# Kernel tuning notes

Hardware: AMD Instinct MI355X
Metric: run time of the kernel (lower is better)

Reference implementation:

```python
import jax, jax.numpy as jnp
import numpy as np
import math

D_MODEL = 768
NUM_HEADS = 12
SPARSITY = 0.7


def setup_inputs() -> dict:
    key = jax.random.key(0)
    ks = jax.random.split(key, 9)
    B, S, D = 2, 2048, D_MODEL
    scale = 1.0 / math.sqrt(D)  # xavier-ish
    inp = {
        "x": jax.random.normal(ks[0], (B, S, D), dtype=jnp.float32),
        "Wq": jax.random.normal(ks[1], (D, D), dtype=jnp.float32) * scale,
        "bq": jnp.zeros((D,), dtype=jnp.float32),
        "Wk": jax.random.normal(ks[2], (D, D), dtype=jnp.float32) * scale,
        "bk": jnp.zeros((D,), dtype=jnp.float32),
        "Wv": jax.random.normal(ks[3], (D, D), dtype=jnp.float32) * scale,
        "bv": jnp.zeros((D,), dtype=jnp.float32),
        "Wo": jax.random.normal(ks[4], (D, D), dtype=jnp.float32) * scale,
        "bo": jnp.zeros((D,), dtype=jnp.float32),
    }
    return inp


def reference(x, Wq, bq, Wk, bk, Wv, bv, Wo, bo):
    B, S, D = x.shape
    H = NUM_HEADS
    hd = D // H
    k_keep = max(1, int((1.0 - SPARSITY) * S))

    # projections (nn.Linear: x @ W.T + b), split into heads -> [B,H,S,hd]
    q = (x @ Wq.T + bq).reshape(B, S, H, hd).transpose(0, 2, 1, 3)
    k = (x @ Wk.T + bk).reshape(B, S, H, hd).transpose(0, 2, 1, 3)
    v = (x @ Wv.T + bv).reshape(B, S, H, hd).transpose(0, 2, 1, 3)

    # dense scores [B,H,S,S]
    scores = jnp.einsum("bhqd,bhkd->bhqk", q, k) / math.sqrt(hd)

    # per-row top-k sparsification (training path of the torch module)
    _, topk_idx = jax.lax.top_k(scores, k_keep)  # [B,H,S,k]
    bi = jnp.arange(B)[:, None, None, None]
    hi = jnp.arange(H)[None, :, None, None]
    si = jnp.arange(S)[None, None, :, None]
    keep = jnp.zeros(scores.shape, dtype=bool).at[bi, hi, si, topk_idx].set(True)
    scores = jnp.where(keep, scores, jnp.float32(-1e9))

    attn = jax.nn.softmax(scores, axis=-1)
    out = jnp.einsum("bhqk,bhkd->bhqd", attn, v)  # [B,H,S,hd]
    out = out.transpose(0, 2, 1, 3).reshape(B, S, D)
    return out @ Wo.T + bo
```

## Files before the change

kernel.cpp:

```cpp
#include <hip/hip_runtime.h>
#include <math.h>

#define B_ 2
#define S_ 2048
#define D_ 768
#define H_ 12
#define HD_ 64
#define KKEEP 614
#define M_ (B_*S_)
#define KD_ 768
#define SRW 2072

typedef __attribute__((ext_vector_type(8))) short bf8;
typedef __attribute__((ext_vector_type(4))) float f4;

__device__ __forceinline__ unsigned short f2bf(float f) {
    unsigned u = __float_as_uint(f);
    u += 0x7FFF + ((u >> 16) & 1);
    return (unsigned short)(u >> 16);
}
__device__ __forceinline__ float bf2f(unsigned short h) {
    return __uint_as_float((unsigned)h << 16);
}
__device__ __forceinline__ unsigned ord16(unsigned short h) {
    return (h & 0x8000u) ? ((~(unsigned)h) & 0xFFFFu) : ((unsigned)h | 0x8000u);
}
__device__ __forceinline__ unsigned short inv16(unsigned o) {
    return (unsigned short)((o & 0x8000u) ? (o & 0x7FFFu) : ((~o) & 0xFFFFu));
}

__global__ void split_kernel(const float* __restrict__ src,
                             unsigned short* __restrict__ hi,
                             unsigned short* __restrict__ lo, int n) {
    int i = blockIdx.x * blockDim.x + threadIdx.x;
    int stride = gridDim.x * blockDim.x;
    for (; i < n; i += stride) {
        float f = src[i];
        unsigned short h = f2bf(f);
        hi[i] = h;
        lo[i] = f2bf(f - bf2f(h));
    }
}

template<int MODE, int WLO>
__global__ __launch_bounds__(256)
void gemm_bf16s(const unsigned short* __restrict__ Ahi, const unsigned short* __restrict__ Alo,
                const unsigned short* __restrict__ Whi, const unsigned short* __restrict__ Wlo,
                const float* __restrict__ bias,
                float* __restrict__ outf,
                unsigned short* __restrict__ ohi, unsigned short* __restrict__ olo) {
    __shared__ unsigned short Ah[128][32], Al[128][32], Bh[64][32], Bl[64][32];
    const int bm = blockIdx.x * 128, bn = blockIdx.y * 64;
    const int tid = threadIdx.x, lane = tid & 63, wave = tid >> 6;
    const int col = lane & 15, quad = lane >> 4;

    f4 acc[2][4];
#pragma unroll
    for (int mi = 0; mi < 2; ++mi)
#pragma unroll
        for (int ni = 0; ni < 4; ++ni) { f4 z = {0.f,0.f,0.f,0.f}; acc[mi][ni] = z; }

    for (int kt = 0; kt < KD_; kt += 32) {
        __syncthreads();
#pragma unroll
        for (int c = 0; c < 2; ++c) {
            int idx = c * 256 + tid;
            int row = idx >> 2, ko = (idx & 3) * 8;
            *(uint4*)&Ah[row][ko] = *(const uint4*)&Ahi[(size_t)(bm + row) * KD_ + kt + ko];
            *(uint4*)&Al[row][ko] = *(const uint4*)&Alo[(size_t)(bm + row) * KD_ + kt + ko];
        }
        {
            int row = tid >> 2, ko = (tid & 3) * 8;
            *(uint4*)&Bh[row][ko] = *(const uint4*)&Whi[(size_t)(bn + row) * KD_ + kt + ko];
            *(uint4*)&Bl[row][ko] = *(const uint4*)&Wlo[(size_t)(bn + row) * KD_ + kt + ko];
        }
        __syncthreads();

        bf8 af[2][2], wf[4][2];
#pragma unroll
        for (int mi = 0; mi < 2; ++mi) {
            int r = wave * 32 + mi * 16 + col;
            af[mi][0] = *(const bf8*)&Ah[r][quad * 8];
            af[mi][1] = *(const bf8*)&Al[r][quad * 8];
        }
#pragma unroll
        for (int ni = 0; ni < 4; ++ni) {
            int r = ni * 16 + col;
            wf[ni][0] = *(const bf8*)&Bh[r][quad * 8];
            wf[ni][1] = *(const bf8*)&Bl[r][quad * 8];
        }
#pragma unroll
        for (int mi = 0; mi < 2; ++mi)
#pragma unroll
            for (int ni = 0; ni < 4; ++ni) {
                acc[mi][ni] = __builtin_amdgcn_mfma_f32_16x16x32_bf16(af[mi][0], wf[ni][0], acc[mi][ni], 0, 0, 0);
                acc[mi][ni] = __builtin_amdgcn_mfma_f32_16x16x32_bf16(af[mi][1], wf[ni][0], acc[mi][ni], 0, 0, 0);
                acc[mi][ni] = __builtin_amdgcn_mfma_f32_16x16x32_bf16(af[mi][0], wf[ni][1], acc[mi][ni], 0, 0, 0);
            }
    }

    float bv[4];
#pragma unroll
    for (int ni = 0; ni < 4; ++ni) bv[ni] = bias[bn + ni * 16 + col];
#pragma unroll
    for (int mi = 0; mi < 2; ++mi)
#pragma unroll
        for (int ni = 0; ni < 4; ++ni)
#pragma unroll
            for (int r = 0; r < 4; ++r) {
                int m = bm + wave * 32 + mi * 16 + quad * 4 + r;
                int n = bn + ni * 16 + col;
                float v = acc[mi][ni][r] + bv[ni];
                if (MODE == 0) {
                    outf[(size_t)m * D_ + n] = v;
                } else {
                    int b = m >> 11, s = m & 2047, h = n >> 6, d = n & 63;
                    size_t idx = (MODE == 1)
                        ? ((((size_t)b * H_ + h) * S_ + s) * HD_ + d)
                        : ((((size_t)b * H_ + h) * HD_ + d) * S_ + s);
                    unsigned short hh = f2bf(v);
                    ohi[idx] = hh;
                    if (WLO) olo[idx] = f2bf(v - bf2f(hh));
                }
            }
}

__global__ __launch_bounds__(1024, 8)
void attn_kernel(const unsigned short* __restrict__ Qhi, const unsigned short* __restrict__ Qlo,
                 const unsigned short* __restrict__ Khi,
                 const unsigned short* __restrict__ Vthi,
                 unsigned short* __restrict__ AOhi, unsigned short* __restrict__ AOlo) {
    const int bid = blockIdx.x;
    const int xcd = bid & 7, sub = (bid >> 3) % 3, tile = bid / 24;
    const int bh = xcd * 3 + sub;
    const int b = bh / H_, h = bh % H_;
    const int q0 = tile * 16;
    const int tid = threadIdx.x, lane = tid & 63, wave = tid >> 6;
    const int col = lane & 15, quad = lane >> 4;

    __shared__ __align__(16) unsigned char arena[16 * 4144];
    unsigned short* scB = (unsigned short*)arena;
    float (*osum)[16][64] = (float (*)[16][64])arena;
    __shared__ float linv[16];

    const size_t qbase = ((size_t)bh * S_ + q0 + col) * HD_;
    bf8 qh0 = *(const bf8*)&Qhi[qbase + quad * 8];
    bf8 qh1 = *(const bf8*)&Qhi[qbase + 32 + quad * 8];
    bf8 ql0 = *(const bf8*)&Qlo[qbase + quad * 8];
    bf8 ql1 = *(const bf8*)&Qlo[qbase + 32 + quad * 8];

    const size_t kbb = (size_t)bh * S_ * HD_;
#pragma unroll
    for (int t = 0; t < 8; ++t) {
        const size_t kr = kbb + (size_t)(wave * 128 + t * 16 + col) * HD_;
        bf8 kh0 = *(const bf8*)&Khi[kr + quad * 8];
        bf8 kh1 = *(const bf8*)&Khi[kr + 32 + quad * 8];
        f4 a = {0.f, 0.f, 0.f, 0.f};
        a = __builtin_amdgcn_mfma_f32_16x16x32_bf16(qh0, kh0, a, 0, 0, 0);
        a = __builtin_amdgcn_mfma_f32_16x16x32_bf16(qh1, kh1, a, 0, 0, 0);
        a = __builtin_amdgcn_mfma_f32_16x16x32_bf16(ql0, kh0, a, 0, 0, 0);
        a = __builtin_amdgcn_mfma_f32_16x16x32_bf16(ql1, kh1, a, 0, 0, 0);
#pragma unroll
        for (int r = 0; r < 4; ++r)
            scB[(quad * 4 + r) * SRW + wave * 128 + t * 16 + col] =
                (unsigned short)ord16(f2bf(a[r] * 0.125f));
    }
    __syncthreads();

    unsigned* rowp = (unsigned*)(arena + wave * 4144);
    unsigned kv[16];
#pragma unroll
    for (int j = 0; j < 16; ++j) kv[j] = rowp[lane + 64 * j];

    unsigned mo = 0;
#pragma unroll
    for (int j = 0; j < 16; ++j) {
        unsigned hi = kv[j] >> 16, lo = kv[j] & 0xFFFFu;
        mo = mo > hi ? mo : hi;
        mo = mo > lo ? mo : lo;
    }
#pragma unroll
    for (int off = 1; off < 64; off <<= 1) {
        unsigned v = __shfl_xor((int)mo, off, 64);
        mo = mo > v ? mo : v;
    }
    unsigned T = 0;
#pragma unroll
    for (int bit = 15; bit >= 0; --bit) {
        unsigned cand = T | (1u << bit);
        int cnt = 0;
#pragma unroll
        for (int j = 0; j < 16; ++j)
            cnt += (int)((kv[j] >> 16) >= cand) + (int)((kv[j] & 0xFFFFu) >= cand);
#pragma unroll
        for (int off = 1; off < 64; off <<= 1) cnt += __shfl_xor(cnt, off, 64);
        if (cnt >= KKEEP) T = cand;
    }
    const float m = bf2f(inv16(mo));

    float ls = 0.f;
#pragma unroll
    for (int j = 0; j < 16; ++j) {
        unsigned v = kv[j];
        unsigned lo = v & 0xFFFFu, hi = v >> 16;
        float wl = (lo >= T) ? __expf(bf2f(inv16(lo)) - m) : 0.f;
        float wh = (hi >= T) ? __expf(bf2f(inv16(hi)) - m) : 0.f;
        ls += wl + wh;
        rowp[lane + 64 * j] = (unsigned)f2bf(wl) | ((unsigned)f2bf(wh) << 16);
    }
#pragma unroll
    for (int off = 1; off < 64; off <<= 1) ls += __shfl_xor(ls, off, 64);
    if (lane == 0) linv[wave] = 1.f / ls;
    __syncthreads();

    f4 od[4];
#pragma unroll
    for (int dt = 0; dt < 4; ++dt) { f4 z = {0.f,0.f,0.f,0.f}; od[dt] = z; }
    const size_t vbb = (size_t)bh * HD_ * S_;
#pragma unroll
    for (int c = 0; c < 4; ++c) {
        bf8 ph = *(const bf8*)&scB[col * SRW + wave * 128 + c * 32 + quad * 8];
        const size_t sbase = (size_t)(wave * 128 + c * 32 + quad * 8);
#pragma unroll
        for (int dt = 0; dt < 4; ++dt) {
            bf8 vh = *(const bf8*)&Vthi[vbb + (size_t)(dt * 16 + col) * S_ + sbase];
            od[dt] = __builtin_amdgcn_mfma_f32_16x16x32_bf16(ph, vh, od[dt], 0, 0, 0);
        }
    }
    __syncthreads();
    if (wave < 8) {
#pragma unroll
        for (int dt = 0; dt < 4; ++dt)
#pragma unroll
            for (int r = 0; r < 4; ++r)
                osum[wave][quad * 4 + r][dt * 16 + col] = od[dt][r];
    }
    __syncthreads();
    if (wave >= 8) {
#pragma unroll
        for (int dt = 0; dt < 4; ++dt)
#pragma unroll
            for (int r = 0; r < 4; ++r)
                osum[wave - 8][quad * 4 + r][dt * 16 + col] += od[dt][r];
    }
    __syncthreads();

    {
        int q = tid >> 6, d = tid & 63;
        float s = 0.f;
#pragma unroll
        for (int w = 0; w < 8; ++w) s += osum[w][q][d];
        s *= linv[q];
        size_t idx = ((size_t)b * S_ + q0 + q) * D_ + h * HD_ + d;
        unsigned short hh = f2bf(s);
        AOhi[idx] = hh;
        AOlo[idx] = f2bf(s - bf2f(hh));
    }
}

extern "C" void kernel_launch(void* const* d_in, const int* in_sizes, int n_in,
                              void* d_out, int out_size, void* d_ws, size_t ws_size,
                              hipStream_t stream) {
    const float* x  = (const float*)d_in[0];
    const float* Wq = (const float*)d_in[1];
    const float* bq = (const float*)d_in[2];
    const float* Wk = (const float*)d_in[3];
    const float* bk = (const float*)d_in[4];
    const float* Wv = (const float*)d_in[5];
    const float* bv = (const float*)d_in[6];
    const float* Wo = (const float*)d_in[7];
    const float* bo = (const float*)d_in[8];
    float* out = (float*)d_out;

    const size_t NP = (size_t)M_ * D_;
    const size_t NW = (size_t)D_ * D_;
    unsigned short* p = (unsigned short*)d_ws;
    unsigned short* xhi = p;  p += NP;
    unsigned short* xlo = p;  p += NP;
    unsigned short* Wqh = p;  p += NW;  unsigned short* Wql = p;  p += NW;
    unsigned short* Wkh = p;  p += NW;  unsigned short* Wkl = p;  p += NW;
    unsigned short* Wvh = p;  p += NW;  unsigned short* Wvl = p;  p += NW;
    unsigned short* Woh = p;  p += NW;  unsigned short* Wol = p;  p += NW;
    unsigned short* Qh  = p;  p += NP;  unsigned short* Ql  = p;  p += NP;
    unsigned short* Kh  = p;  p += NP;  unsigned short* Kl  = p;  p += NP;
    unsigned short* Vth = p;  p += NP;  unsigned short* Vtl = p;  p += NP;
    unsigned short* AOh = xhi;
    unsigned short* AOl = xlo;

    split_kernel<<<(int)((NP + 255) / 256), 256, 0, stream>>>(x,  xhi, xlo, (int)NP);
    split_kernel<<<(int)((NW + 255) / 256), 256, 0, stream>>>(Wq, Wqh, Wql, (int)NW);
    split_kernel<<<(int)((NW + 255) / 256), 256, 0, stream>>>(Wk, Wkh, Wkl, (int)NW);
    split_kernel<<<(int)((NW + 255) / 256), 256, 0, stream>>>(Wv, Wvh, Wvl, (int)NW);
    split_kernel<<<(int)((NW + 255) / 256), 256, 0, stream>>>(Wo, Woh, Wol, (int)NW);

    dim3 g(M_ / 128, D_ / 64);
    gemm_bf16s<1, 1><<<g, 256, 0, stream>>>(xhi, xlo, Wqh, Wql, bq, nullptr, Qh, Ql);
    gemm_bf16s<1, 0><<<g, 256, 0, stream>>>(xhi, xlo, Wkh, Wkl, bk, nullptr, Kh, Kl);
    gemm_bf16s<2, 0><<<g, 256, 0, stream>>>(xhi, xlo, Wvh, Wvl, bv, nullptr, Vth, Vtl);

    attn_kernel<<<(S_ / 16) * B_ * H_, 1024, 0, stream>>>(Qh, Ql, Kh, Vth, AOh, AOl);

    gemm_bf16s<0, 0><<<g, 256, 0, stream>>>(AOh, AOl, Woh, Wol, bo, out, nullptr, nullptr);
}
```

Measured before the change: 469.6 us.

## Fuse QKV projections into one GEMM launch and batch weight splits

Merges the three Q/K/V projection GEMMs into a single launch over a concatenated weight buffer, with the output routing chosen per block. The four weight hi/lo split kernels become one 2D-grid launch. Several loops in the attention kernel change from full unrolling to `#pragma unroll 1`, probably to cut register pressure at 1024 threads per block. The aim is to remove launch overhead and fill the GPU better in the projection phase, at the risk of slower rolled loops in attention.

```diff
diff --git a/kernel.cpp b/kernel.cpp
--- a/kernel.cpp
+++ b/kernel.cpp
@@ -33,24 +33,39 @@
                              unsigned short* __restrict__ hi,
                              unsigned short* __restrict__ lo, int n) {
     int i = blockIdx.x * blockDim.x + threadIdx.x;
-    int stride = gridDim.x * blockDim.x;
-    for (; i < n; i += stride) {
-        float f = src[i];
-        unsigned short h = f2bf(f);
-        hi[i] = h;
-        lo[i] = f2bf(f - bf2f(h));
-    }
-}
-
-template<int MODE, int WLO>
+    if (i >= n) return;
+    float f = src[i];
+    unsigned short h = f2bf(f);
+    hi[i] = h;
+    lo[i] = f2bf(f - bf2f(h));
+}
+
+__global__ void split_w_kernel(const float* __restrict__ w0, const float* __restrict__ w1,
+                               const float* __restrict__ w2, const float* __restrict__ w3,
+                               unsigned short* __restrict__ hi,
+                               unsigned short* __restrict__ lo) {
+    const int which = blockIdx.y;
+    const float* src = which == 0 ? w0 : (which == 1 ? w1 : (which == 2 ? w2 : w3));
+    int i = blockIdx.x * blockDim.x + threadIdx.x;
+    size_t o = (size_t)which * (D_ * D_) + i;
+    float f = src[i];
+    unsigned short h = f2bf(f);
+    hi[o] = h;
+    lo[o] = f2bf(f - bf2f(h));
+}
+
 __global__ __launch_bounds__(256)
-void gemm_bf16s(const unsigned short* __restrict__ Ahi, const unsigned short* __restrict__ Alo,
-                const unsigned short* __restrict__ Whi, const unsigned short* __restrict__ Wlo,
-                const float* __restrict__ bias,
-                float* __restrict__ outf,
-                unsigned short* __restrict__ ohi, unsigned short* __restrict__ olo) {
+void gemm_qkv(const unsigned short* __restrict__ Ahi, const unsigned short* __restrict__ Alo,
+              const unsigned short* __restrict__ Wch, const unsigned short* __restrict__ Wcl,
+              const float* __restrict__ bq, const float* __restrict__ bk,
+              const float* __restrict__ bv,
+              unsigned short* __restrict__ Qh, unsigned short* __restrict__ Ql,
+              unsigned short* __restrict__ Kh, unsigned short* __restrict__ Vth) {
     __shared__ unsigned short Ah[128][32], Al[128][32], Bh[64][32], Bl[64][32];
-    const int bm = blockIdx.x * 128, bn = blockIdx.y * 64;
+    const int bm = blockIdx.x * 128, bnG = blockIdx.y * 64;
+    const int which = blockIdx.y / 12;
+    const int bn = bnG - which * 768;
+    const float* bias = which == 0 ? bq : (which == 1 ? bk : bv);
     const int tid = threadIdx.x, lane = tid & 63, wave = tid >> 6;
     const int col = lane & 15, quad = lane >> 4;
 
@@ -71,8 +86,8 @@
         }
         {
             int row = tid >> 2, ko = (tid & 3) * 8;
-            *(uint4*)&Bh[row][ko] = *(const uint4*)&Whi[(size_t)(bn + row) * KD_ + kt + ko];
-            *(uint4*)&Bl[row][ko] = *(const uint4*)&Wlo[(size_t)(bn + row) * KD_ + kt + ko];
+            *(uint4*)&Bh[row][ko] = *(const uint4*)&Wch[(size_t)(bnG + row) * KD_ + kt + ko];
+            *(uint4*)&Bl[row][ko] = *(const uint4*)&Wcl[(size_t)(bnG + row) * KD_ + kt + ko];
         }
         __syncthreads();
 
@@ -99,9 +114,9 @@
             }
     }
 
-    float bv[4];
-#pragma unroll
-    for (int ni = 0; ni < 4; ++ni) bv[ni] = bias[bn + ni * 16 + col];
+    float bvv[4];
+#pragma unroll
+    for (int ni = 0; ni < 4; ++ni) bvv[ni] = bias[bn + ni * 16 + col];
 #pragma unroll
     for (int mi = 0; mi < 2; ++mi)
 #pragma unroll
@@ -110,18 +125,87 @@
             for (int r = 0; r < 4; ++r) {
                 int m = bm + wave * 32 + mi * 16 + quad * 4 + r;
                 int n = bn + ni * 16 + col;
-                float v = acc[mi][ni][r] + bv[ni];
-                if (MODE == 0) {
-                    outf[(size_t)m * D_ + n] = v;
+                float v = acc[mi][ni][r] + bvv[ni];
+                int b = m >> 11, s = m & 2047, h = n >> 6, d = n & 63;
+                unsigned short hh = f2bf(v);
+                if (which == 0) {
+                    size_t idx = (((size_t)b * H_ + h) * S_ + s) * HD_ + d;
+                    Qh[idx] = hh;
+                    Ql[idx] = f2bf(v - bf2f(hh));
+                } else if (which == 1) {
+                    Kh[(((size_t)b * H_ + h) * S_ + s) * HD_ + d] = hh;
                 } else {
-                    int b = m >> 11, s = m & 2047, h = n >> 6, d = n & 63;
-                    size_t idx = (MODE == 1)
-                        ? ((((size_t)b * H_ + h) * S_ + s) * HD_ + d)
-                        : ((((size_t)b * H_ + h) * HD_ + d) * S_ + s);
-                    unsigned short hh = f2bf(v);
-                    ohi[idx] = hh;
-                    if (WLO) olo[idx] = f2bf(v - bf2f(hh));
+                    Vth[(((size_t)b * H_ + h) * HD_ + d) * S_ + s] = hh;
                 }
+            }
+}
+
+__global__ __launch_bounds__(256)
+void gemm_o(const unsigned short* __restrict__ Ahi, const unsigned short* __restrict__ Alo,
+            const unsigned short* __restrict__ Whi, const unsigned short* __restrict__ Wlo,
+            const float* __restrict__ bias, float* __restrict__ outf) {
+    __shared__ unsigned short Ah[128][32], Al[128][32], Bh[64][32], Bl[64][32];
+    const int bm = blockIdx.x * 128, bn = blockIdx.y * 64;
+    const int tid = threadIdx.x, lane = tid & 63, wave = tid >> 6;
+    const int col = lane & 15, quad = lane >> 4;
+
+    f4 acc[2][4];
+#pragma unroll
+    for (int mi = 0; mi < 2; ++mi)
+#pragma unroll
+        for (int ni = 0; ni < 4; ++ni) { f4 z = {0.f,0.f,0.f,0.f}; acc[mi][ni] = z; }
+
+    for (int kt = 0; kt < KD_; kt += 32) {
+        __syncthreads();
+#pragma unroll
+        for (int c = 0; c < 2; ++c) {
+            int idx = c * 256 + tid;
+            int row = idx >> 2, ko = (idx & 3) * 8;
+            *(uint4*)&Ah[row][ko] = *(const uint4*)&Ahi[(size_t)(bm + row) * KD_ + kt + ko];
+            *(uint4*)&Al[row][ko] = *(const uint4*)&Alo[(size_t)(bm + row) * KD_ + kt + ko];
+        }
+        {
+            int row = tid >> 2, ko = (tid & 3) * 8;
+            *(uint4*)&Bh[row][ko] = *(const uint4*)&Whi[(size_t)(bn + row) * KD_ + kt + ko];
+            *(uint4*)&Bl[row][ko] = *(const uint4*)&Wlo[(size_t)(bn + row) * KD_ + kt + ko];
+        }
+        __syncthreads();
+
+        bf8 af[2][2], wf[4][2];
+#pragma unroll
+        for (int mi = 0; mi < 2; ++mi) {
+            int r = wave * 32 + mi * 16 + col;
+            af[mi][0] = *(const bf8*)&Ah[r][quad * 8];
+            af[mi][1] = *(const bf8*)&Al[r][quad * 8];
+        }
+#pragma unroll
+        for (int ni = 0; ni < 4; ++ni) {
+            int r = ni * 16 + col;
+            wf[ni][0] = *(const bf8*)&Bh[r][quad * 8];
+            wf[ni][1] = *(const bf8*)&Bl[r][quad * 8];
+        }
+#pragma unroll
+        for (int mi = 0; mi < 2; ++mi)
+#pragma unroll
+            for (int ni = 0; ni < 4; ++ni) {
+                acc[mi][ni] = __builtin_amdgcn_mfma_f32_16x16x32_bf16(af[mi][0], wf[ni][0], acc[mi][ni], 0, 0, 0);
+                acc[mi][ni] = __builtin_amdgcn_mfma_f32_16x16x32_bf16(af[mi][1], wf[ni][0], acc[mi][ni], 0, 0, 0);
+                acc[mi][ni] = __builtin_amdgcn_mfma_f32_16x16x32_bf16(af[mi][0], wf[ni][1], acc[mi][ni], 0, 0, 0);
+            }
+    }
+
+    float bvv[4];
+#pragma unroll
+    for (int ni = 0; ni < 4; ++ni) bvv[ni] = bias[bn + ni * 16 + col];
+#pragma unroll
+    for (int mi = 0; mi < 2; ++mi)
+#pragma unroll
+        for (int ni = 0; ni < 4; ++ni)
+#pragma unroll
+            for (int r = 0; r < 4; ++r) {
+                int m = bm + wave * 32 + mi * 16 + quad * 4 + r;
+                int n = bn + ni * 16 + col;
+                outf[(size_t)m * D_ + n] = acc[mi][ni][r] + bvv[ni];
             }
 }
 
@@ -150,7 +234,7 @@
     bf8 ql1 = *(const bf8*)&Qlo[qbase + 32 + quad * 8];
 
     const size_t kbb = (size_t)bh * S_ * HD_;
-#pragma unroll
+#pragma unroll 1
     for (int t = 0; t < 8; ++t) {
         const size_t kr = kbb + (size_t)(wave * 128 + t * 16 + col) * HD_;
         bf8 kh0 = *(const bf8*)&Khi[kr + quad * 8];
@@ -185,7 +269,7 @@
         mo = mo > v ? mo : v;
     }
     unsigned T = 0;
-#pragma unroll
+#pragma unroll 1
     for (int bit = 15; bit >= 0; --bit) {
         unsigned cand = T | (1u << bit);
         int cnt = 0;
@@ -199,7 +283,7 @@
     const float m = bf2f(inv16(mo));
 
     float ls = 0.f;
-#pragma unroll
+#pragma unroll 1
     for (int j = 0; j < 16; ++j) {
         unsigned v = kv[j];
         unsigned lo = v & 0xFFFFu, hi = v >> 16;
@@ -217,7 +301,7 @@
 #pragma unroll
     for (int dt = 0; dt < 4; ++dt) { f4 z = {0.f,0.f,0.f,0.f}; od[dt] = z; }
     const size_t vbb = (size_t)bh * HD_ * S_;
-#pragma unroll
+#pragma unroll 1
     for (int c = 0; c < 4; ++c) {
         bf8 ph = *(const bf8*)&scB[col * SRW + wave * 128 + c * 32 + quad * 8];
         const size_t sbase = (size_t)(wave * 128 + c * 32 + quad * 8);
@@ -277,28 +361,30 @@
     unsigned short* p = (unsigned short*)d_ws;
     unsigned short* xhi = p;  p += NP;
     unsigned short* xlo = p;  p += NP;
-    unsigned short* Wqh = p;  p += NW;  unsigned short* Wql = p;  p += NW;
-    unsigned short* Wkh = p;  p += NW;  unsigned short* Wkl = p;  p += NW;
-    unsigned short* Wvh = p;  p += NW;  unsigned short* Wvl = p;  p += NW;
-    unsigned short* Woh = p;  p += NW;  unsigned short* Wol = p;  p += NW;
+    unsigned short* Wch = p;  p += 4 * NW;
+    unsigned short* Wcl = p;  p += 4 * NW;
     unsigned short* Qh  = p;  p += NP;  unsigned short* Ql  = p;  p += NP;
-    unsigned short* Kh  = p;  p += NP;  unsigned short* Kl  = p;  p += NP;
-    unsigned short* Vth = p;  p += NP;  unsigned short* Vtl = p;  p += NP;
+    unsigned short* Kh  = p;  p += NP;
+    unsigned short* Vth = p;  p += NP;
     unsigned short* AOh = xhi;
     unsigned short* AOl = xlo;
 
-    split_kernel<<<(int)((NP + 255) / 256), 256, 0, stream>>>(x,  xhi, xlo, (int)NP);
-    split_kernel<<<(int)((NW + 255) / 256), 256, 0, stream>>>(Wq, Wqh, Wql, (int)NW);
-    split_kernel<<<(int)((NW + 255) / 256), 256, 0, stream>>>(Wk, Wkh, Wkl, (int)NW);
-    split_kernel<<<(int)((NW + 255) / 256), 256, 0, stream>>>(Wv, Wvh, Wvl, (int)NW);
-    split_kernel<<<(int)((NW + 255) / 256), 256, 0, stream>>>(Wo, Woh, Wol, (int)NW);
-
-    dim3 g(M_ / 128, D_ / 64);
-    gemm_bf16s<1, 1><<<g, 256, 0, stream>>>(xhi, xlo, Wqh, Wql, bq, nullptr, Qh, Ql);
-    gemm_bf16s<1, 0><<<g, 256, 0, stream>>>(xhi, xlo, Wkh, Wkl, bk, nullptr, Kh, Kl);
-    gemm_bf16s<2, 0><<<g, 256, 0, stream>>>(xhi, xlo, Wvh, Wvl, bv, nullptr, Vth, Vtl);
+    split_kernel<<<(int)(NP / 256), 256, 0, stream>>>(x, xhi, xlo, (int)NP);
+    {
+        dim3 gw((unsigned)(NW / 256), 4);
+        split_w_kernel<<<gw, 256, 0, stream>>>(Wq, Wk, Wv, Wo, Wch, Wcl);
+    }
+
+    {
+        dim3 g(M_ / 128, 36);
+        gemm_qkv<<<g, 256, 0, stream>>>(xhi, xlo, Wch, Wcl, bq, bk, bv,
+                                        Qh, Ql, Kh, Vth);
+    }
 
     attn_kernel<<<(S_ / 16) * B_ * H_, 1024, 0, stream>>>(Qh, Ql, Kh, Vth, AOh, AOl);
 
-    gemm_bf16s<0, 0><<<g, 256, 0, stream>>>(AOh, AOl, Woh, Wol, bo, out, nullptr, nullptr);
-}
+    {
+        dim3 g(M_ / 128, D_ / 64);
+        gemm_o<<<g, 256, 0, stream>>>(AOh, AOl, Wch + 3 * NW, Wcl + 3 * NW, bo, out);
+    }
+}
```

After: 439.9 us. 6.3% less time.
